# Optimization experiments

Hardware: AMD Instinct MI355X
Metric: run time of the kernel (lower is better)

## Reference

```python
import jax, jax.numpy as jnp
import numpy as np

H, W = 720, 1280
FX, FY = 800.0, 800.0
CX, CY = 640.0, 360.0
N_POINTS = 4000000


def setup_inputs() -> dict:
    key = jax.random.key(0)
    k1, k2, k3 = jax.random.split(key, 3)
    positions = jax.random.normal(k1, (N_POINTS, 3), jnp.float32) * 0.05 \
        + jnp.array([0.0, 0.0, 0.5], jnp.float32)
    scales = jnp.ones((N_POINTS, 3), jnp.float32) * 0.01
    colors = jax.random.uniform(k2, (N_POINTS, 3), jnp.float32)
    camera_poses = jax.random.normal(k3, (4, 4, 4), jnp.float32)  # unused by the math
    return {"camera_poses": camera_poses, "positions": positions,
            "scales": scales, "colors": colors}


def reference(camera_poses, positions, scales, colors):
    # Pinhole projection (camera_poses is ignored by the original module).
    x = positions[:, 0]
    y = positions[:, 1]
    z = positions[:, 2] + 3.0
    u = FX * (x / z) + CX  # [N]
    v = FY * (y / z) + CY  # [N]

    valid = (u >= 0) & (u < W) & (v >= 0) & (v < H)

    xi = jnp.floor(u)
    yi = jnp.floor(v)
    dx = u - xi  # fractional offsets (original: x - int(x))
    dy = v - yi
    radius = scales[:, 0] * 100.0
    weight = jnp.exp(-(dx * dx + dy * dy) / (2.0 * radius * radius))  # [N]

    # Flat pixel id; invalid points go to a dummy extra segment.
    pix = yi.astype(jnp.int32) * W + xi.astype(jnp.int32)
    pix = jnp.where(valid, pix, H * W)

    n = positions.shape[0]
    winner = jax.ops.segment_max(jnp.arange(n, dtype=jnp.int32), pix,
                                 num_segments=H * W + 1)[: H * W]
    has_point = winner >= 0  # empty segments get int32 min
    idx = jnp.clip(winner, 0, n - 1)

    pix_color = colors[idx] * weight[idx][:, None]  # [H*W, 3]
    img = jnp.where(has_point[:, None], pix_color, jnp.float32(0.0))
    return img.reshape(H, W, 3)
```

## Files before the change

### kernel.cpp

```cpp
#include <hip/hip_runtime.h>

#define IMG_H 720
#define IMG_W 1280
#define FX_C 800.0f
#define FY_C 800.0f
#define CX_C 640.0f
#define CY_C 360.0f

#define WIN_W 96
#define WIN_H 96
#define WIN_X0 (640 - WIN_W / 2)
#define WIN_Y0 (360 - WIN_H / 2)
#define WIN_PIX (WIN_W * WIN_H)
#define LDS_STRIDE 97
#define NGROUPS 32
#define SCAT_BLOCKS 256
#define SCAT_THREADS 512

__global__ __launch_bounds__(256) void init_winner_kernel(int4* __restrict__ winner4,
                                                          int nquads) {
    int stride = gridDim.x * blockDim.x;
    for (int i = blockIdx.x * blockDim.x + threadIdx.x; i < nquads; i += stride)
        winner4[i] = make_int4(-1, -1, -1, -1);
}

__device__ __forceinline__ void project_point(float x, float y, float zraw,
                                              float& u, float& v) {
    float z = __fadd_rn(zraw, 3.0f);
    u = __fadd_rn(__fmul_rn(FX_C, __fdiv_rn(x, z)), CX_C);
    v = __fadd_rn(__fmul_rn(FY_C, __fdiv_rn(y, z)), CY_C);
}

__device__ __forceinline__ void splat_one(int i, float x, float y, float zraw,
                                          int* lwin, int* __restrict__ winner) {
    float u, v;
    project_point(x, y, zraw, u, v);
    if (u >= 0.0f && u < (float)IMG_W && v >= 0.0f && v < (float)IMG_H) {
        int xi = (int)floorf(u);
        int yi = (int)floorf(v);
        int wx = xi - WIN_X0;
        int wy = yi - WIN_Y0;
        if ((unsigned)wx < WIN_W && (unsigned)wy < WIN_H) {
            atomicMax(&lwin[wy * LDS_STRIDE + wx], i);
        } else {
            int pix = yi * IMG_W + xi;
            if (winner[pix] < i) atomicMax(&winner[pix], i);
        }
    }
}

__global__ __launch_bounds__(SCAT_THREADS) void scatter_win_kernel(
        const float* __restrict__ pos, int* __restrict__ winner,
        int* __restrict__ blockwin, int n, int per_block) {
    __shared__ int lwin[WIN_H * LDS_STRIDE];
    for (int j = threadIdx.x; j < WIN_H * LDS_STRIDE; j += SCAT_THREADS) lwin[j] = -1;
    __syncthreads();

    int base = blockIdx.x * per_block;
    int end  = base + per_block;
    if (end > n) end = n;

    #pragma unroll 2
    for (int i0 = base + (int)threadIdx.x * 4; i0 < end; i0 += SCAT_THREADS * 4) {
        if (i0 + 4 <= end) {
            const float4* p4 = (const float4*)(pos + 3 * i0);
            float4 a = p4[0], b = p4[1], c = p4[2];
            splat_one(i0 + 0, a.x, a.y, a.z, lwin, winner);
            splat_one(i0 + 1, a.w, b.x, b.y, lwin, winner);
            splat_one(i0 + 2, b.z, b.w, c.x, lwin, winner);
            splat_one(i0 + 3, c.y, c.z, c.w, lwin, winner);
        } else {
            for (int i = i0; i < end; ++i)
                splat_one(i, pos[3 * i], pos[3 * i + 1], pos[3 * i + 2], lwin, winner);
        }
    }
    __syncthreads();

    int* dst = blockwin + (size_t)blockIdx.x * WIN_PIX;
    for (int j = threadIdx.x; j < WIN_PIX; j += SCAT_THREADS) {
        int wy = j / WIN_W;
        int wx = j - wy * WIN_W;
        dst[j] = lwin[wy * LDS_STRIDE + wx];
    }
}

__global__ __launch_bounds__(256) void reduce1_kernel(
        const int* __restrict__ blockwin, int* __restrict__ part2,
        int nblocks, int gsize) {
    int g = blockIdx.x;
    int p = blockIdx.y * 256 + threadIdx.x;
    int b0 = g * gsize;
    int b1 = b0 + gsize; if (b1 > nblocks) b1 = nblocks;
    int m = -1;
    for (int b = b0; b < b1; ++b) {
        int v = blockwin[(size_t)b * WIN_PIX + p];
        m = v > m ? v : m;
    }
    part2[(size_t)g * WIN_PIX + p] = m;
}

__global__ void scatter_simple_kernel(const float* __restrict__ pos,
                                      int* __restrict__ winner, int n) {
    int gid = blockIdx.x * blockDim.x + threadIdx.x;
    if (gid >= n) return;
    int i = n - 1 - gid;
    float u, v;
    project_point(pos[3 * i], pos[3 * i + 1], pos[3 * i + 2], u, v);
    if (u >= 0.0f && u < (float)IMG_W && v >= 0.0f && v < (float)IMG_H) {
        int pix = (int)floorf(v) * IMG_W + (int)floorf(u);
        if (winner[pix] < i) atomicMax(&winner[pix], i);
    }
}

__global__ __launch_bounds__(256) void resolve_kernel(
        const float* __restrict__ pos, const float* __restrict__ scales,
        const float* __restrict__ colors, const int* __restrict__ part2,
        const int* __restrict__ winner, float* __restrict__ out,
        int npix, int use_part2) {
    int p = blockIdx.x * blockDim.x + threadIdx.x;
    if (p >= npix) return;
    int py = p / IMG_W;
    int px = p - py * IMG_W;
    int wx = px - WIN_X0;
    int wy = py - WIN_Y0;
    int w;
    if (use_part2 && (unsigned)wx < WIN_W && (unsigned)wy < WIN_H) {
        int wp = wy * WIN_W + wx;
        int m = -1;
        #pragma unroll
        for (int g = 0; g < NGROUPS; ++g) {
            int v = part2[g * WIN_PIX + wp];
            m = v > m ? v : m;
        }
        w = m;
    } else {
        w = winner[p];
    }
    float cr = 0.0f, cg = 0.0f, cb = 0.0f;
    if (w >= 0) {
        float u, v;
        project_point(pos[3 * w], pos[3 * w + 1], pos[3 * w + 2], u, v);
        float dx = __fsub_rn(u, floorf(u));
        float dy = __fsub_rn(v, floorf(v));
        float rad = __fmul_rn(scales[3 * w], 100.0f);
        float num = __fadd_rn(__fmul_rn(dx, dx), __fmul_rn(dy, dy));
        float den = __fmul_rn(2.0f, __fmul_rn(rad, rad));
        float wgt = expf(-__fdiv_rn(num, den));
        cr = __fmul_rn(colors[3 * w + 0], wgt);
        cg = __fmul_rn(colors[3 * w + 1], wgt);
        cb = __fmul_rn(colors[3 * w + 2], wgt);
    }
    out[3 * p + 0] = cr;
    out[3 * p + 1] = cg;
    out[3 * p + 2] = cb;
}

extern "C" void kernel_launch(void* const* d_in, const int* in_sizes, int n_in,
                              void* d_out, int out_size, void* d_ws, size_t ws_size,
                              hipStream_t stream) {
    const float* positions = (const float*)d_in[1];
    const float* scales    = (const float*)d_in[2];
    const float* colors    = (const float*)d_in[3];
    float* out = (float*)d_out;
    int n = in_sizes[1] / 3;
    const int npix = IMG_H * IMG_W;

    const size_t winner_bytes = (size_t)npix * sizeof(int);
    const size_t part2_bytes  = (size_t)NGROUPS * WIN_PIX * sizeof(int);
    const size_t slice_bytes  = (size_t)WIN_PIX * sizeof(int);

    int* winner = (int*)d_ws;

    init_winner_kernel<<<900, 256, 0, stream>>>((int4*)winner, npix / 4);

    long long avail = (long long)ws_size - (long long)winner_bytes - (long long)part2_bytes;
    int nblocks = (avail > 0) ? (int)(avail / (long long)slice_bytes) : 0;
    if (nblocks > SCAT_BLOCKS) nblocks = SCAT_BLOCKS;

    if (nblocks >= 128) {
        int* part2    = (int*)((char*)d_ws + winner_bytes);
        int* blockwin = (int*)((char*)d_ws + winner_bytes + part2_bytes);
        int per_block = ((n + nblocks - 1) / nblocks + 3) & ~3;
        int gsize = (nblocks + NGROUPS - 1) / NGROUPS;

        scatter_win_kernel<<<nblocks, SCAT_THREADS, 0, stream>>>(positions, winner,
                                                                 blockwin, n, per_block);
        dim3 g1(NGROUPS, WIN_PIX / 256);
        reduce1_kernel<<<g1, 256, 0, stream>>>(blockwin, part2, nblocks, gsize);
        resolve_kernel<<<(npix + 255) / 256, 256, 0, stream>>>(
            positions, scales, colors, part2, winner, out, npix, 1);
    } else {
        scatter_simple_kernel<<<(n + 255) / 256, 256, 0, stream>>>(positions, winner, n);
        resolve_kernel<<<(npix + 255) / 256, 256, 0, stream>>>(
            positions, scales, colors, (const int*)d_ws , winner, out, npix, 0);
    }
}
```

Before: 30.85 us.

## Fuse init, scatter, reduce and resolve into one cooperative kernel

Replaces the four-launch pipeline (init, windowed scatter, partial reduce, resolve) with a single cooperative kernel that uses grid-wide syncs between phases. The block size doubles to 1024 threads and the number of reduction groups drops from 32 to 16. The aim is to cut launch overhead and gaps between kernels. In exchange, every phase now runs on only 256 blocks, and grid.sync adds its own cost, which may hurt the memory-bound resolve phase.

```diff
diff --git a/kernel.cpp b/kernel.cpp
--- a/kernel.cpp
+++ b/kernel.cpp
@@ -1,7 +1,11 @@
 #include <hip/hip_runtime.h>
+#include <hip/hip_cooperative_groups.h>
+
+namespace cg = cooperative_groups;
 
 #define IMG_H 720
 #define IMG_W 1280
+#define NPIX (IMG_H * IMG_W)
 #define FX_C 800.0f
 #define FY_C 800.0f
 #define CX_C 640.0f
@@ -13,16 +17,10 @@
 #define WIN_Y0 (360 - WIN_H / 2)
 #define WIN_PIX (WIN_W * WIN_H)
 #define LDS_STRIDE 97
-#define NGROUPS 32
-#define SCAT_BLOCKS 256
-#define SCAT_THREADS 512
-
-__global__ __launch_bounds__(256) void init_winner_kernel(int4* __restrict__ winner4,
-                                                          int nquads) {
-    int stride = gridDim.x * blockDim.x;
-    for (int i = blockIdx.x * blockDim.x + threadIdx.x; i < nquads; i += stride)
-        winner4[i] = make_int4(-1, -1, -1, -1);
-}
+
+#define NBLK 256
+#define NTHR 1024
+#define NR 16
 
 __device__ __forceinline__ void project_point(float x, float y, float zraw,
                                               float& u, float& v) {
@@ -49,19 +47,29 @@
     }
 }
 
-__global__ __launch_bounds__(SCAT_THREADS) void scatter_win_kernel(
-        const float* __restrict__ pos, int* __restrict__ winner,
-        int* __restrict__ blockwin, int n, int per_block) {
+__global__ __launch_bounds__(NTHR) void fused_kernel(
+        const float* __restrict__ pos, const float* __restrict__ scales,
+        const float* __restrict__ colors, int* __restrict__ winner,
+        int* __restrict__ blockwin, int* __restrict__ part16,
+        float* __restrict__ out, int n, int per_block) {
+    cg::grid_group grid = cg::this_grid();
     __shared__ int lwin[WIN_H * LDS_STRIDE];
-    for (int j = threadIdx.x; j < WIN_H * LDS_STRIDE; j += SCAT_THREADS) lwin[j] = -1;
-    __syncthreads();
+
+    const int tid = blockIdx.x * NTHR + (int)threadIdx.x;
+    const int nthreads = NBLK * NTHR;
+
+    int4* w4 = (int4*)winner;
+    for (int i = tid; i < NPIX / 4; i += nthreads)
+        w4[i] = make_int4(-1, -1, -1, -1);
+    for (int j = threadIdx.x; j < WIN_H * LDS_STRIDE; j += NTHR)
+        lwin[j] = -1;
+    grid.sync();
 
     int base = blockIdx.x * per_block;
     int end  = base + per_block;
     if (end > n) end = n;
 
-    #pragma unroll 2
-    for (int i0 = base + (int)threadIdx.x * 4; i0 < end; i0 += SCAT_THREADS * 4) {
+    for (int i0 = base + (int)threadIdx.x * 4; i0 < end; i0 += NTHR * 4) {
         if (i0 + 4 <= end) {
             const float4* p4 = (const float4*)(pos + 3 * i0);
             float4 a = p4[0], b = p4[1], c = p4[2];
@@ -76,27 +84,73 @@
     }
     __syncthreads();
 
-    int* dst = blockwin + (size_t)blockIdx.x * WIN_PIX;
-    for (int j = threadIdx.x; j < WIN_PIX; j += SCAT_THREADS) {
-        int wy = j / WIN_W;
-        int wx = j - wy * WIN_W;
-        dst[j] = lwin[wy * LDS_STRIDE + wx];
-    }
-}
-
-__global__ __launch_bounds__(256) void reduce1_kernel(
-        const int* __restrict__ blockwin, int* __restrict__ part2,
-        int nblocks, int gsize) {
-    int g = blockIdx.x;
-    int p = blockIdx.y * 256 + threadIdx.x;
-    int b0 = g * gsize;
-    int b1 = b0 + gsize; if (b1 > nblocks) b1 = nblocks;
-    int m = -1;
-    for (int b = b0; b < b1; ++b) {
-        int v = blockwin[(size_t)b * WIN_PIX + p];
-        m = v > m ? v : m;
-    }
-    part2[(size_t)g * WIN_PIX + p] = m;
+    {
+        int* dst = blockwin + (size_t)blockIdx.x * WIN_PIX;
+        for (int j = threadIdx.x; j < WIN_PIX; j += NTHR) {
+            int wy = j / WIN_W;
+            int wx = j - wy * WIN_W;
+            dst[j] = lwin[wy * LDS_STRIDE + wx];
+        }
+    }
+    grid.sync();
+
+    for (int t = tid; t < NR * WIN_PIX; t += nthreads) {
+        int g = t / WIN_PIX;
+        int p = t - g * WIN_PIX;
+        const int* src = blockwin + (size_t)(g * (NBLK / NR)) * WIN_PIX + p;
+        int m = -1;
+        #pragma unroll
+        for (int b = 0; b < NBLK / NR; ++b) {
+            int v = src[(size_t)b * WIN_PIX];
+            m = v > m ? v : m;
+        }
+        part16[t] = m;
+    }
+    grid.sync();
+
+    for (int p = tid; p < NPIX; p += nthreads) {
+        int py = p / IMG_W;
+        int px = p - py * IMG_W;
+        int wx = px - WIN_X0;
+        int wy = py - WIN_Y0;
+        int w;
+        if ((unsigned)wx < WIN_W && (unsigned)wy < WIN_H) {
+            int wp = wy * WIN_W + wx;
+            int m = -1;
+            #pragma unroll
+            for (int g = 0; g < NR; ++g) {
+                int v = part16[g * WIN_PIX + wp];
+                m = v > m ? v : m;
+            }
+            w = m;
+        } else {
+            w = winner[p];
+        }
+        float cr = 0.0f, cgr = 0.0f, cb = 0.0f;
+        if (w >= 0) {
+            float u, v;
+            project_point(pos[3 * w], pos[3 * w + 1], pos[3 * w + 2], u, v);
+            float dx = __fsub_rn(u, floorf(u));
+            float dy = __fsub_rn(v, floorf(v));
+            float rad = __fmul_rn(scales[3 * w], 100.0f);
+            float num = __fadd_rn(__fmul_rn(dx, dx), __fmul_rn(dy, dy));
+            float den = __fmul_rn(2.0f, __fmul_rn(rad, rad));
+            float wgt = expf(-__fdiv_rn(num, den));
+            cr  = __fmul_rn(colors[3 * w + 0], wgt);
+            cgr = __fmul_rn(colors[3 * w + 1], wgt);
+            cb  = __fmul_rn(colors[3 * w + 2], wgt);
+        }
+        out[3 * p + 0] = cr;
+        out[3 * p + 1] = cgr;
+        out[3 * p + 2] = cb;
+    }
+}
+
+__global__ __launch_bounds__(256) void init_winner_kernel(int4* __restrict__ winner4,
+                                                          int nquads) {
+    int stride = gridDim.x * blockDim.x;
+    for (int i = blockIdx.x * blockDim.x + threadIdx.x; i < nquads; i += stride)
+        winner4[i] = make_int4(-1, -1, -1, -1);
 }
 
 __global__ void scatter_simple_kernel(const float* __restrict__ pos,
@@ -112,31 +166,14 @@
     }
 }
 
-__global__ __launch_bounds__(256) void resolve_kernel(
+__global__ __launch_bounds__(256) void resolve_simple_kernel(
         const float* __restrict__ pos, const float* __restrict__ scales,
-        const float* __restrict__ colors, const int* __restrict__ part2,
-        const int* __restrict__ winner, float* __restrict__ out,
-        int npix, int use_part2) {
+        const float* __restrict__ colors, const int* __restrict__ winner,
+        float* __restrict__ out, int npix) {
     int p = blockIdx.x * blockDim.x + threadIdx.x;
     if (p >= npix) return;
-    int py = p / IMG_W;
-    int px = p - py * IMG_W;
-    int wx = px - WIN_X0;
-    int wy = py - WIN_Y0;
-    int w;
-    if (use_part2 && (unsigned)wx < WIN_W && (unsigned)wy < WIN_H) {
-        int wp = wy * WIN_W + wx;
-        int m = -1;
-        #pragma unroll
-        for (int g = 0; g < NGROUPS; ++g) {
-            int v = part2[g * WIN_PIX + wp];
-            m = v > m ? v : m;
-        }
-        w = m;
-    } else {
-        w = winner[p];
-    }
-    float cr = 0.0f, cg = 0.0f, cb = 0.0f;
+    int w = winner[p];
+    float cr = 0.0f, cgr = 0.0f, cb = 0.0f;
     if (w >= 0) {
         float u, v;
         project_point(pos[3 * w], pos[3 * w + 1], pos[3 * w + 2], u, v);
@@ -146,12 +183,12 @@
         float num = __fadd_rn(__fmul_rn(dx, dx), __fmul_rn(dy, dy));
         float den = __fmul_rn(2.0f, __fmul_rn(rad, rad));
         float wgt = expf(-__fdiv_rn(num, den));
-        cr = __fmul_rn(colors[3 * w + 0], wgt);
-        cg = __fmul_rn(colors[3 * w + 1], wgt);
-        cb = __fmul_rn(colors[3 * w + 2], wgt);
+        cr  = __fmul_rn(colors[3 * w + 0], wgt);
+        cgr = __fmul_rn(colors[3 * w + 1], wgt);
+        cb  = __fmul_rn(colors[3 * w + 2], wgt);
     }
     out[3 * p + 0] = cr;
-    out[3 * p + 1] = cg;
+    out[3 * p + 1] = cgr;
     out[3 * p + 2] = cb;
 }
 
@@ -163,35 +200,27 @@
     const float* colors    = (const float*)d_in[3];
     float* out = (float*)d_out;
     int n = in_sizes[1] / 3;
-    const int npix = IMG_H * IMG_W;
-
-    const size_t winner_bytes = (size_t)npix * sizeof(int);
-    const size_t part2_bytes  = (size_t)NGROUPS * WIN_PIX * sizeof(int);
-    const size_t slice_bytes  = (size_t)WIN_PIX * sizeof(int);
+
+    const size_t winner_bytes   = (size_t)NPIX * sizeof(int);
+    const size_t part16_bytes   = (size_t)NR * WIN_PIX * sizeof(int);
+    const size_t blockwin_bytes = (size_t)NBLK * WIN_PIX * sizeof(int);
 
     int* winner = (int*)d_ws;
 
-    init_winner_kernel<<<900, 256, 0, stream>>>((int4*)winner, npix / 4);
-
-    long long avail = (long long)ws_size - (long long)winner_bytes - (long long)part2_bytes;
-    int nblocks = (avail > 0) ? (int)(avail / (long long)slice_bytes) : 0;
-    if (nblocks > SCAT_BLOCKS) nblocks = SCAT_BLOCKS;
-
-    if (nblocks >= 128) {
-        int* part2    = (int*)((char*)d_ws + winner_bytes);
-        int* blockwin = (int*)((char*)d_ws + winner_bytes + part2_bytes);
-        int per_block = ((n + nblocks - 1) / nblocks + 3) & ~3;
-        int gsize = (nblocks + NGROUPS - 1) / NGROUPS;
-
-        scatter_win_kernel<<<nblocks, SCAT_THREADS, 0, stream>>>(positions, winner,
-                                                                 blockwin, n, per_block);
-        dim3 g1(NGROUPS, WIN_PIX / 256);
-        reduce1_kernel<<<g1, 256, 0, stream>>>(blockwin, part2, nblocks, gsize);
-        resolve_kernel<<<(npix + 255) / 256, 256, 0, stream>>>(
-            positions, scales, colors, part2, winner, out, npix, 1);
+    if (ws_size >= winner_bytes + part16_bytes + blockwin_bytes) {
+        int* part16   = (int*)((char*)d_ws + winner_bytes);
+        int* blockwin = (int*)((char*)d_ws + winner_bytes + part16_bytes);
+        int per_block = ((n + NBLK - 1) / NBLK + 3) & ~3;
+
+        void* args[] = { (void*)&positions, (void*)&scales, (void*)&colors,
+                         (void*)&winner, (void*)&blockwin, (void*)&part16,
+                         (void*)&out, (void*)&n, (void*)&per_block };
+        hipLaunchCooperativeKernel((const void*)fused_kernel,
+                                   dim3(NBLK), dim3(NTHR), args, 0, stream);
     } else {
+        init_winner_kernel<<<900, 256, 0, stream>>>((int4*)winner, NPIX / 4);
         scatter_simple_kernel<<<(n + 255) / 256, 256, 0, stream>>>(positions, winner, n);
-        resolve_kernel<<<(npix + 255) / 256, 256, 0, stream>>>(
-            positions, scales, colors, (const int*)d_ws , winner, out, npix, 0);
-    }
-}
+        resolve_simple_kernel<<<(NPIX + 255) / 256, 256, 0, stream>>>(
+            positions, scales, colors, winner, out, NPIX);
+    }
+}
```

New measurement: 113.2 us. 267% more time.

## Fuse window reduction into resolve kernel, dropping the intermediate reduce pass

Applied to the files above, without the earlier changes.

Removes the separate two-stage reduction kernel. The first 36 blocks of the resolve kernel now reduce all 256 per-block window slices directly and shade the window pixels, while the remaining blocks handle the other pixels. This saves one kernel launch and the part2 round trip. The cost is that 36 blocks each run a long serial 256-deep strided read, so the tail may be limited by those few blocks. The init kernel also switches to one thread per quad.

```diff
diff --git a/kernel.cpp b/kernel.cpp
--- a/kernel.cpp
+++ b/kernel.cpp
@@ -2,6 +2,7 @@
 
 #define IMG_H 720
 #define IMG_W 1280
+#define NPIX (IMG_H * IMG_W)
 #define FX_C 800.0f
 #define FY_C 800.0f
 #define CX_C 640.0f
@@ -13,15 +14,15 @@
 #define WIN_Y0 (360 - WIN_H / 2)
 #define WIN_PIX (WIN_W * WIN_H)
 #define LDS_STRIDE 97
-#define NGROUPS 32
+
 #define SCAT_BLOCKS 256
 #define SCAT_THREADS 512
+#define RBLK 36
 
 __global__ __launch_bounds__(256) void init_winner_kernel(int4* __restrict__ winner4,
                                                           int nquads) {
-    int stride = gridDim.x * blockDim.x;
-    for (int i = blockIdx.x * blockDim.x + threadIdx.x; i < nquads; i += stride)
-        winner4[i] = make_int4(-1, -1, -1, -1);
+    int i = blockIdx.x * blockDim.x + threadIdx.x;
+    if (i < nquads) winner4[i] = make_int4(-1, -1, -1, -1);
 }
 
 __device__ __forceinline__ void project_point(float x, float y, float zraw,
@@ -84,19 +85,70 @@
     }
 }
 
-__global__ __launch_bounds__(256) void reduce1_kernel(
-        const int* __restrict__ blockwin, int* __restrict__ part2,
-        int nblocks, int gsize) {
-    int g = blockIdx.x;
-    int p = blockIdx.y * 256 + threadIdx.x;
-    int b0 = g * gsize;
-    int b1 = b0 + gsize; if (b1 > nblocks) b1 = nblocks;
-    int m = -1;
-    for (int b = b0; b < b1; ++b) {
-        int v = blockwin[(size_t)b * WIN_PIX + p];
-        m = v > m ? v : m;
+__device__ __forceinline__ void shade_and_store(
+        const float* __restrict__ pos, const float* __restrict__ scales,
+        const float* __restrict__ colors, float* __restrict__ out, int p, int w) {
+    float cr = 0.0f, cgr = 0.0f, cb = 0.0f;
+    if (w >= 0) {
+        float u, v;
+        project_point(pos[3 * w], pos[3 * w + 1], pos[3 * w + 2], u, v);
+        float dx = __fsub_rn(u, floorf(u));
+        float dy = __fsub_rn(v, floorf(v));
+        float rad = __fmul_rn(scales[3 * w], 100.0f);
+        float num = __fadd_rn(__fmul_rn(dx, dx), __fmul_rn(dy, dy));
+        float den = __fmul_rn(2.0f, __fmul_rn(rad, rad));
+        float wgt = expf(-__fdiv_rn(num, den));
+        cr  = __fmul_rn(colors[3 * w + 0], wgt);
+        cgr = __fmul_rn(colors[3 * w + 1], wgt);
+        cb  = __fmul_rn(colors[3 * w + 2], wgt);
     }
-    part2[(size_t)g * WIN_PIX + p] = m;
+    out[3 * p + 0] = cr;
+    out[3 * p + 1] = cgr;
+    out[3 * p + 2] = cb;
+}
+
+__global__ __launch_bounds__(256) void resolve_kernel(
+        const float* __restrict__ pos, const float* __restrict__ scales,
+        const float* __restrict__ colors, const int* __restrict__ blockwin,
+        const int* __restrict__ winner, float* __restrict__ out,
+        int npix, int nblocks_scat, int use_blockwin) {
+    if (use_blockwin && blockIdx.x < RBLK) {
+        int wp = blockIdx.x * 256 + threadIdx.x;
+        const int* src = blockwin + wp;
+        int m0 = -1, m1 = -1, m2 = -1, m3 = -1;
+        int b = 0;
+        for (; b + 4 <= nblocks_scat; b += 4) {
+            int v0 = src[(size_t)(b + 0) * WIN_PIX];
+            int v1 = src[(size_t)(b + 1) * WIN_PIX];
+            int v2 = src[(size_t)(b + 2) * WIN_PIX];
+            int v3 = src[(size_t)(b + 3) * WIN_PIX];
+            m0 = v0 > m0 ? v0 : m0;
+            m1 = v1 > m1 ? v1 : m1;
+            m2 = v2 > m2 ? v2 : m2;
+            m3 = v3 > m3 ? v3 : m3;
+        }
+        for (; b < nblocks_scat; ++b) {
+            int v = src[(size_t)b * WIN_PIX];
+            m0 = v > m0 ? v : m0;
+        }
+        int m = m0 > m1 ? m0 : m1;
+        int mb = m2 > m3 ? m2 : m3;
+        m = m > mb ? m : mb;
+        int wy = wp / WIN_W;
+        int wx = wp - wy * WIN_W;
+        int p = (WIN_Y0 + wy) * IMG_W + (WIN_X0 + wx);
+        shade_and_store(pos, scales, colors, out, p, m);
+        return;
+    }
+    int p = (blockIdx.x - (use_blockwin ? RBLK : 0)) * 256 + (int)threadIdx.x;
+    if (p >= npix) return;
+    if (use_blockwin) {
+        int py = p / IMG_W;
+        int px = p - py * IMG_W;
+        if ((unsigned)(px - WIN_X0) < WIN_W && (unsigned)(py - WIN_Y0) < WIN_H)
+            return;
+    }
+    shade_and_store(pos, scales, colors, out, p, winner[p]);
 }
 
 __global__ void scatter_simple_kernel(const float* __restrict__ pos,
@@ -112,49 +164,6 @@
     }
 }
 
-__global__ __launch_bounds__(256) void resolve_kernel(
-        const float* __restrict__ pos, const float* __restrict__ scales,
-        const float* __restrict__ colors, const int* __restrict__ part2,
-        const int* __restrict__ winner, float* __restrict__ out,
-        int npix, int use_part2) {
-    int p = blockIdx.x * blockDim.x + threadIdx.x;
-    if (p >= npix) return;
-    int py = p / IMG_W;
-    int px = p - py * IMG_W;
-    int wx = px - WIN_X0;
-    int wy = py - WIN_Y0;
-    int w;
-    if (use_part2 && (unsigned)wx < WIN_W && (unsigned)wy < WIN_H) {
-        int wp = wy * WIN_W + wx;
-        int m = -1;
-        #pragma unroll
-        for (int g = 0; g < NGROUPS; ++g) {
-            int v = part2[g * WIN_PIX + wp];
-            m = v > m ? v : m;
-        }
-        w = m;
-    } else {
-        w = winner[p];
-    }
-    float cr = 0.0f, cg = 0.0f, cb = 0.0f;
-    if (w >= 0) {
-        float u, v;
-        project_point(pos[3 * w], pos[3 * w + 1], pos[3 * w + 2], u, v);
-        float dx = __fsub_rn(u, floorf(u));
-        float dy = __fsub_rn(v, floorf(v));
-        float rad = __fmul_rn(scales[3 * w], 100.0f);
-        float num = __fadd_rn(__fmul_rn(dx, dx), __fmul_rn(dy, dy));
-        float den = __fmul_rn(2.0f, __fmul_rn(rad, rad));
-        float wgt = expf(-__fdiv_rn(num, den));
-        cr = __fmul_rn(colors[3 * w + 0], wgt);
-        cg = __fmul_rn(colors[3 * w + 1], wgt);
-        cb = __fmul_rn(colors[3 * w + 2], wgt);
-    }
-    out[3 * p + 0] = cr;
-    out[3 * p + 1] = cg;
-    out[3 * p + 2] = cb;
-}
-
 extern "C" void kernel_launch(void* const* d_in, const int* in_sizes, int n_in,
                               void* d_out, int out_size, void* d_ws, size_t ws_size,
                               hipStream_t stream) {
@@ -163,35 +172,26 @@
     const float* colors    = (const float*)d_in[3];
     float* out = (float*)d_out;
     int n = in_sizes[1] / 3;
-    const int npix = IMG_H * IMG_W;
 
-    const size_t winner_bytes = (size_t)npix * sizeof(int);
-    const size_t part2_bytes  = (size_t)NGROUPS * WIN_PIX * sizeof(int);
-    const size_t slice_bytes  = (size_t)WIN_PIX * sizeof(int);
+    const size_t winner_bytes   = (size_t)NPIX * sizeof(int);
+    const size_t blockwin_bytes = (size_t)SCAT_BLOCKS * WIN_PIX * sizeof(int);
 
     int* winner = (int*)d_ws;
 
-    init_winner_kernel<<<900, 256, 0, stream>>>((int4*)winner, npix / 4);
+    init_winner_kernel<<<NPIX / 4 / 256, 256, 0, stream>>>((int4*)winner, NPIX / 4);
 
-    long long avail = (long long)ws_size - (long long)winner_bytes - (long long)part2_bytes;
-    int nblocks = (avail > 0) ? (int)(avail / (long long)slice_bytes) : 0;
-    if (nblocks > SCAT_BLOCKS) nblocks = SCAT_BLOCKS;
+    if (ws_size >= winner_bytes + blockwin_bytes) {
+        int* blockwin = (int*)((char*)d_ws + winner_bytes);
+        int per_block = ((n + SCAT_BLOCKS - 1) / SCAT_BLOCKS + 3) & ~3;
 
-    if (nblocks >= 128) {
-        int* part2    = (int*)((char*)d_ws + winner_bytes);
-        int* blockwin = (int*)((char*)d_ws + winner_bytes + part2_bytes);
-        int per_block = ((n + nblocks - 1) / nblocks + 3) & ~3;
-        int gsize = (nblocks + NGROUPS - 1) / NGROUPS;
-
-        scatter_win_kernel<<<nblocks, SCAT_THREADS, 0, stream>>>(positions, winner,
-                                                                 blockwin, n, per_block);
-        dim3 g1(NGROUPS, WIN_PIX / 256);
-        reduce1_kernel<<<g1, 256, 0, stream>>>(blockwin, part2, nblocks, gsize);
-        resolve_kernel<<<(npix + 255) / 256, 256, 0, stream>>>(
-            positions, scales, colors, part2, winner, out, npix, 1);
+        scatter_win_kernel<<<SCAT_BLOCKS, SCAT_THREADS, 0, stream>>>(
+            positions, winner, blockwin, n, per_block);
+        resolve_kernel<<<RBLK + (NPIX + 255) / 256, 256, 0, stream>>>(
+            positions, scales, colors, blockwin, winner, out, NPIX, SCAT_BLOCKS, 1);
     } else {
         scatter_simple_kernel<<<(n + 255) / 256, 256, 0, stream>>>(positions, winner, n);
-        resolve_kernel<<<(npix + 255) / 256, 256, 0, stream>>>(
-            positions, scales, colors, (const int*)d_ws , winner, out, npix, 0);
+        resolve_kernel<<<(NPIX + 255) / 256, 256, 0, stream>>>(
+            positions, scales, colors, (const int*)winner , winner, out,
+            NPIX, 0, 0);
     }
 }
```

Result: slower. 37.67 us (+22.1%).
